# Performance work log

Measured on AMD Instinct MI355X. Metric: run time of the kernel, lower is better.

The kernel has to match this reference:

```python
import jax, jax.numpy as jnp
import numpy as np

IMG = 640
STRIDES = (8, 16, 32)
A = 5            # anchors per level
NC = 80          # num classes
IOU_TH = 0.5
NEG_RATIO = 1.0


def make_priors():
    scales = [1.0, 1.5, 2.0, 2.5, 3.0]
    out = []
    for s in STRIDES:
        f = IMG // s
        ys, xs = np.meshgrid(np.arange(f), np.arange(f), indexing='ij')
        cx = ((xs + 0.5) / f).ravel()
        cy = ((ys + 0.5) / f).ravel()
        for sc in scales:  # anchor-major to match merge_features (A, h, w) order
            wh = min(sc * 4.0 * s / IMG, 1.0)
            out.append(np.stack([cx, cy, np.full_like(cx, wh), np.full_like(cx, wh)], 1))
    return np.concatenate(out, 0).astype(np.float32)  # [42000, 4] cxcywh


def merge_features(feats):
    outs = []
    for feat in feats:
        n, c, h, w = feat.shape
        f = feat.reshape(n, A, c // A, h, w).transpose(0, 1, 3, 4, 2)
        outs.append(f.reshape(n, A * h * w, c // A))
    return jnp.concatenate(outs, axis=1)  # [n, M, 85]


def box_iou_cxcywh(a, b):
    # a [T,4], b [M,4] (cx,cy,w,h) -> IoU [T,M]
    a1 = jnp.concatenate([a[:, :2] - a[:, 2:] / 2, a[:, :2] + a[:, 2:] / 2], -1)
    b1 = jnp.concatenate([b[:, :2] - b[:, 2:] / 2, b[:, :2] + b[:, 2:] / 2], -1)
    tl = jnp.maximum(a1[:, None, :2], b1[None, :, :2])
    br = jnp.minimum(a1[:, None, 2:], b1[None, :, 2:])
    wh = jnp.clip(br - tl, 0.0)
    inter = wh[..., 0] * wh[..., 1]
    area_a = a[:, 2] * a[:, 3]
    area_b = b[:, 2] * b[:, 3]
    return inter / (area_a[:, None] + area_b[None, :] - inter + 1e-9)


def build_targets(targets, priors, batch):
    ious = box_iou_cxcywh(targets[:, 2:6], priors)  # [Nt, M]
    Nt, M = ious.shape
    img_ids = targets[:, 0].astype(jnp.int32)

    def per_image(i):
        valid = img_ids == i  # [Nt]
        iv = jnp.where(valid[:, None], ious, -1.0)
        best_gt_overlap = iv.max(0)            # [M]
        best_gt_idx = iv.argmax(0)             # [M]
        best_prior_idx = iv.argmax(1)          # [Nt]
        # torch: index_fill_(1) then sequential best_gt_overlap[best_prior_idx[j]] = j
        local_j = (jnp.cumsum(valid.astype(jnp.int32)) - 1).astype(jnp.float32)
        scat_idx = jnp.where(valid, best_prior_idx, M)  # drop invalid rows
        best_gt_overlap = best_gt_overlap.at[scat_idx].set(local_j, mode='drop')
        bbox = targets[best_gt_idx, 2:6]
        clss = targets[best_gt_idx, 1] + 1.0
        clss = jnp.where(best_gt_overlap < IOU_TH, 0.0, clss)
        t_xy = (bbox[:, :2] - priors[:, :2]) / priors[:, 2:]
        t_wh = jnp.log(bbox[:, 2:] / priors[:, 2:])
        return t_xy, t_wh, clss

    return jax.vmap(per_image)(jnp.arange(batch))  # [B,M,2],[B,M,2],[B,M]


def _smooth_l1(x):
    ax = jnp.abs(x)
    return jnp.where(ax < 1.0, 0.5 * ax * ax, ax - 0.5)


def compute_loss(preds, priors, targets):
    n, m, _ = preds.shape
    t_xy, t_wh, t_cls = build_targets(targets, priors, n)
    pos = t_cls > 0
    posf = pos.astype(preds.dtype)
    num_pos = posf.sum()

    # lbox: smooth L1 on xy and wh over positives (mean over pos*2 elements each)
    den2 = jnp.maximum(num_pos * 2.0, 1.0)
    lbox = (_smooth_l1(preds[..., 0:2] - t_xy) * posf[..., None]).sum() / den2 \
         + (_smooth_l1(preds[..., 2:4] - t_wh) * posf[..., None]).sum() / den2

    # lcls: cross entropy over positives, labels = t_cls - 1
    labels = jnp.clip(t_cls.astype(jnp.int32) - 1, 0, NC - 1)
    logz = jax.nn.log_softmax(preds[..., 5:], axis=-1)
    ce = -jnp.take_along_axis(logz, labels[..., None], axis=-1)[..., 0]
    lcls = (ce * posf).sum() / jnp.maximum(num_pos, 1.0)

    # hard negative mining (no grad): double argsort rank trick
    obj = preds[..., 4]
    loss_c = jax.lax.stop_gradient(-jax.nn.log_sigmoid(obj))
    loss_c = jnp.where(pos, 0.0, loss_c)
    order = jnp.argsort(-loss_c, axis=-1)
    rank = jnp.argsort(order, axis=-1)
    num_neg = jnp.minimum(NEG_RATIO * num_pos, m - num_pos)
    neg = rank.astype(preds.dtype) < num_neg
    sel = (pos | neg).astype(preds.dtype)

    # lobj: BCE-with-logits over pos|neg
    z = posf
    bce = jnp.maximum(obj, 0.0) - obj * z + jnp.log1p(jnp.exp(-jnp.abs(obj)))
    lobj = (bce * sel).sum() / jnp.maximum(sel.sum(), 1.0)

    loss = lbox + lcls + lobj
    return jnp.stack([loss, lbox, lobj, lcls])


def setup_inputs() -> dict:
    key = jax.random.key(0)
    ks = jax.random.split(key, 6)
    feat0 = jax.random.normal(ks[0], (8, 425, 80, 80), jnp.float32)
    feat1 = jax.random.normal(ks[1], (8, 425, 40, 40), jnp.float32)
    feat2 = jax.random.normal(ks[2], (8, 425, 20, 20), jnp.float32)
    B, T = 8, 20
    img = jnp.repeat(jnp.arange(B, dtype=jnp.float32), T)
    cls = jax.random.randint(ks[3], (B * T,), 0, NC).astype(jnp.float32)
    cxcy = jax.random.uniform(ks[4], (B * T, 2), minval=0.2, maxval=0.8)
    wh = jax.random.uniform(ks[5], (B * T, 2), minval=0.05, maxval=0.3)
    targets = jnp.concatenate([img[:, None], cls[:, None], cxcy, wh], 1)
    priors = jnp.asarray(make_priors())
    return {"feat0": feat0, "feat1": feat1, "feat2": feat2,
            "targets": targets, "priors": priors}


def reference(feat0, feat1, feat2, targets, priors):
    preds = merge_features([feat0, feat1, feat2])  # [8, 42000, 85]
    return compute_loss(preds, priors, targets)    # [loss, lbox, lobj, lcls]
```

## Files before the change

kernel.cpp:

```cpp
#include <hip/hip_runtime.h>
#include <math.h>

#define MTOT 42000
#define NB 8
#define NCLS 80
#define CAP_LIST 4096
#define NT_MAX 2048
#define GX_MAIN 165
#define NBLK_MAIN (GX_MAIN*NB)
#define NCHB 8
#define CSB 5250
#define TCH 512
#define TST 384

#define O_OVR 0
#define O_GIX (O_OVR + NB*MTOT*4)
#define O_LSC (O_GIX + NB*MTOT*4)
#define O_BCE (O_LSC + NB*MTOT*4)
#define O_LJ  (O_BCE + NB*MTOT*4)
#define O_BPP (((O_LJ + NT_MAX*4 + 7)/8)*8)
#define O_HP  (O_BPP + NT_MAX*NCHB*8)
#define O_HD  (O_HP + NBLK_MAIN*256*4)
#define O_PA  (O_HD + NB*256*4)
#define O_PN  (O_PA + NBLK_MAIN*16)
#define O_P2  (O_PN + NBLK_MAIN*4)
#define O_BINL (O_P2 + NBLK_MAIN*8)
#define O_HB  (((O_BINL + NB*CAP_LIST*2*4 + 255)/256)*256)
#define O_ACCI (O_HB + NB*256*4)
#define O_ZEND (O_ACCI + 128)
#define ZWORDS ((O_ZEND - O_HB)/4)
#define ZBLK ((ZWORDS + 255)/256)

__device__ __forceinline__ float iou_cxcywh(float acx,float acy,float aw,float ah,
                                            float bcx,float bcy,float bw,float bh){
  float ax0=acx-aw*0.5f, ay0=acy-ah*0.5f, ax1=acx+aw*0.5f, ay1=acy+ah*0.5f;
  float bx0=bcx-bw*0.5f, by0=bcy-bh*0.5f, bx1=bcx+bw*0.5f, by1=bcy+bh*0.5f;
  float tlx=fmaxf(ax0,bx0), tly=fmaxf(ay0,by0);
  float brx=fminf(ax1,bx1), bry=fminf(ay1,by1);
  float wx=fmaxf(brx-tlx,0.f), wy=fmaxf(bry-tly,0.f);
  float inter=wx*wy;
  return inter/(aw*ah+bw*bh-inter+1e-9f);
}

__device__ __forceinline__ float sl1(float x){
  float ax=fabsf(x); return ax<1.f ? 0.5f*ax*ax : ax-0.5f;
}

__device__ __forceinline__ void feat_base(const float* f0,const float* f1,const float* f2,
                                          int i,int m,const float** basep,int* hwp){
  const float* fp; int hw, loc;
  if(m<32000){ fp=f0; hw=6400; loc=m; }
  else if(m<40000){ fp=f1; hw=1600; loc=m-32000; }
  else { fp=f2; hw=400; loc=m-40000; }
  int a=loc/hw, p=loc-a*hw;
  *basep = fp + (size_t)(i*425 + a*85)*(size_t)hw + p;
  *hwp = hw;
}

__device__ __forceinline__ void fine_scan(const unsigned* hb,int ca,int kres,int* bs_out,int* r_out){
  if(ca==0x7fffffff){ *bs_out=0x7fffffff; *r_out=0; return; }
  int run=0, bs=-1, r=0;
  for(int f=255;f>=0;f--){
    int cb=(int)hb[f];
    if(run<kres && run+cb>=kres){ bs=(ca<<8)|f; r=kres-run; break; }
    run+=cb;
  }
  if(bs<0){ bs=(ca<<8); r=kres-run; }
  *bs_out=bs; *r_out=r;
}

__global__ void k_big0(const float* __restrict__ f0,const float* __restrict__ f1,const float* __restrict__ f2,
                       const float* __restrict__ tg,const float* __restrict__ priors,
                       int nt,int b0,int b1,
                       int* __restrict__ lj,unsigned* __restrict__ zbase,
                       float* __restrict__ ovr,int* __restrict__ gix,
                       float* __restrict__ lsc,float* __restrict__ bcearr,
                       unsigned* __restrict__ histP,int* __restrict__ partN,
                       unsigned long long* __restrict__ bpp){
  __shared__ float st[TCH*6];
  __shared__ float sc[TCH*4];
  __shared__ int cidx[TCH];
  __shared__ int s_ncomp;
  __shared__ unsigned long long su[256];
  __shared__ unsigned h[256];
  __shared__ int snp[4];
  int b=blockIdx.x, tid=threadIdx.x, lane=tid&63, wid=tid>>6;
  if(b<ZBLK){
    int w=b*256+tid;
    if(w<ZWORDS) zbase[w]=0u;
    return;
  }
  if(b<b0){
    int t=(b-ZBLK)*256+tid;
    if(t>=nt) return;
    int img=(int)tg[t*6];
    int j=0;
    for(int q=0;q<t;q++) if((int)tg[q*6]==img) j++;
    lj[t]=j;
    return;
  }
  if(b<b1){
    int idx=b-b0;
    int i=idx/GX_MAIN, cb=idx-(idx/GX_MAIN)*GX_MAIN;
    int m=cb*256+tid;
    bool valid=(m<MTOT);
    h[tid]=0u;
    const float* basep=f0; int hw=6400;
    float obj=0.f;
    if(valid){ feat_base(f0,f1,f2,i,m,&basep,&hw); obj=basep[(size_t)4*hw]; }
    float4 pr=make_float4(0.f,0.f,1.f,1.f);
    if(valid) pr=((const float4*)priors)[m];
    float maxv=-1.f; int bi=0;
    for(int base=0;base<nt;base+=TCH){
      int nch=min(TCH,nt-base);
      for(int j=tid;j<nch;j+=256){
        #pragma unroll
        for(int q=0;q<6;q++) st[j*6+q]=tg[(base+j)*6+q];
      }
      __syncthreads();
      if(tid<64){
        int cnt=0;
        for(int bb=0;bb<nch;bb+=64){
          int j=bb+tid;
          bool f=(j<nch)&&((int)st[j*6]==i);
          unsigned long long mk=__ballot(f);
          if(f){
            int pos=cnt+__popcll(mk&((1ull<<tid)-1ull));
            cidx[pos]=base+j;
            sc[pos*4+0]=st[j*6+2]; sc[pos*4+1]=st[j*6+3];
            sc[pos*4+2]=st[j*6+4]; sc[pos*4+3]=st[j*6+5];
          }
          cnt+=__popcll(mk);
        }
        if(tid==0) s_ncomp=cnt;
      }
      __syncthreads();
      int nci=s_ncomp;
      if(valid){
        for(int j=0;j<nci;j++){
          float v=iou_cxcywh(sc[j*4+0],sc[j*4+1],sc[j*4+2],sc[j*4+3],pr.x,pr.y,pr.z,pr.w);
          if(v>maxv){ maxv=v; bi=cidx[j]; }
        }
      }
      __syncthreads();
    }
    int npos=0;
    if(valid){
      int gid=i*MTOT+m;
      ovr[gid]=maxv; gix[gid]=bi;
      int gi=min(max(bi,0),nt-1);
      float tc=tg[gi*6+1]+1.f;
      bool pos=(maxv>=0.5f)&&(tc>0.f);
      float sp=log1pf(expf(-fabsf(obj)));
      float bce=fmaxf(obj,0.f)-(pos?obj:0.f)+sp;
      float lc=pos?0.f:(fmaxf(-obj,0.f)+sp);
      lsc[gid]=lc; bcearr[gid]=bce;
      atomicAdd(&h[__float_as_uint(lc)>>24],1u);
      npos=pos?1:0;
    }
    #pragma unroll
    for(int o=32;o>0;o>>=1) npos+=__shfl_xor(npos,o);
    if(lane==0) snp[wid]=npos;
    __syncthreads();
    histP[(size_t)idx*256+tid]=h[tid];
    if(tid==0) partN[idx]=snp[0]+snp[1]+snp[2]+snp[3];
  } else {
    int idx=b-b1;
    int t=idx/NCHB, c=idx-(idx/NCHB)*NCHB;
    float acx=tg[t*6+2],acy=tg[t*6+3],aw=tg[t*6+4],ah=tg[t*6+5];
    int m0=c*CSB, m1=min(m0+CSB,MTOT);
    float bv=-1.f; int bm=0;
    for(int m=m0+tid;m<m1;m+=256){
      float4 pr=((const float4*)priors)[m];
      float v=iou_cxcywh(acx,acy,aw,ah,pr.x,pr.y,pr.z,pr.w);
      if(v>bv){ bv=v; bm=m; }
    }
    unsigned long long p=(bv<0.f)?0ull
        :(((unsigned long long)__float_as_uint(bv))<<32)|(unsigned)(~bm);
    su[tid]=p;
    __syncthreads();
    for(int o=128;o>0;o>>=1){
      if(tid<o){ if(su[tid+o]>su[tid]) su[tid]=su[tid+o]; }
      __syncthreads();
    }
    if(tid==0) bpp[(size_t)t*NCHB+c]=su[0];
  }
}

__global__ void k_bpsc(const float* __restrict__ f0,const float* __restrict__ f1,const float* __restrict__ f2,
                       const float* __restrict__ tg,int nt,
                       const unsigned long long* __restrict__ bpp,
                       const int* __restrict__ lj,
                       float* __restrict__ ovr,const int* __restrict__ gix,
                       float* __restrict__ lsc,float* __restrict__ bcearr,
                       int* __restrict__ histD,int* __restrict__ acci){
  __shared__ int tbp[NT_MAX];
  __shared__ int timg[NT_MAX];
  __shared__ int hd[NB*256];
  __shared__ int npd;
  int tid=threadIdx.x;
  for(int e=tid;e<NB*256;e+=256) hd[e]=0;
  if(tid==0) npd=0;
  for(int t=tid;t<nt;t+=256){
    unsigned long long best=0ull;
    const unsigned long long* pp=&bpp[(size_t)t*NCHB];
    #pragma unroll
    for(int c=0;c<NCHB;c++){ unsigned long long v=pp[c]; if(v>best) best=v; }
    int bm=~((unsigned)(best&0xFFFFFFFFull));
    tbp[t]=min(max(bm,0),MTOT-1);
    timg[t]=(int)tg[t*6];
  }
  __syncthreads();
  for(int t=tid;t<nt;t+=256){
    int img=timg[t];
    if(img<0||img>=NB) continue;
    int myp=tbp[t];
    bool last=true;
    for(int q=t+1;q<nt;q++) if(timg[q]==img&&tbp[q]==myp){ last=false; break; }
    if(!last) continue;
    int gid=img*MTOT+myp;
    float ljv=(float)lj[t];
    float ov_old=ovr[gid];
    ovr[gid]=ljv;
    int gi=min(max(gix[gid],0),nt-1);
    float tc=tg[gi*6+1]+1.f;
    bool po=(ov_old>=0.5f)&&(tc>0.f);
    bool pn=(ljv>=0.5f)&&(tc>0.f);
    const float* basep; int hw;
    feat_base(f0,f1,f2,img,myp,&basep,&hw);
    float obj=basep[(size_t)4*hw];
    float sp=log1pf(expf(-fabsf(obj)));
    float bcen=fmaxf(obj,0.f)-(pn?obj:0.f)+sp;
    float lcn=pn?0.f:(fmaxf(-obj,0.f)+sp);
    float lco=lsc[gid];
    lsc[gid]=lcn; bcearr[gid]=bcen;
    atomicAdd(&hd[img*256+(int)(__float_as_uint(lco)>>24)],-1);
    atomicAdd(&hd[img*256+(int)(__float_as_uint(lcn)>>24)], 1);
    atomicAdd(&npd,(pn?1:0)-(po?1:0));
  }
  __syncthreads();
  for(int e=tid;e<NB*256;e+=256) histD[e]=hd[e];
  if(tid==0) acci[26]=npd;
}

__global__ void k_big2(const float* __restrict__ f0,const float* __restrict__ f1,const float* __restrict__ f2,
                       const float* __restrict__ tg,const float* __restrict__ priors,
                       const float* __restrict__ ovr,const int* __restrict__ gix,
                       const float* __restrict__ lsc,const float* __restrict__ bcearr,
                       const int* __restrict__ partN,const unsigned* __restrict__ histP,
                       const int* __restrict__ histD,int* __restrict__ acci,int nt,
                       unsigned* __restrict__ histB,float4* __restrict__ partA){
  __shared__ int an[256];
  __shared__ int hc[256];
  __shared__ unsigned hf[256];
  __shared__ int s_ca;
  __shared__ float rA[4],rB[4],rC[4],rD[4];
  int b=blockIdx.x, tid=threadIdx.x, lane=tid&63, wid=tid>>6;
  if(b<NBLK_MAIN){
    int i=b/GX_MAIN, cb=b-(b/GX_MAIN)*GX_MAIN;
    int n=0;
    for(int e=tid;e<NBLK_MAIN;e+=256) n+=partN[e];
    an[tid]=n;
    __syncthreads();
    for(int o=128;o>0;o>>=1){ if(tid<o) an[tid]+=an[tid+o]; __syncthreads(); }
    int np=an[0]+acci[26];
    int cbn=histD[i*256+tid];
    for(int blk=0;blk<GX_MAIN;blk++) cbn+=(int)histP[(size_t)(i*GX_MAIN+blk)*256+tid];
    hc[tid]=cbn;
    __syncthreads();
    if(tid==0){
      int kk=min(np,MTOT-np);
      int ca,kres;
      if(kk<=0){ ca=0x7fffffff; kres=0; }
      else{
        int run=0; ca=-1; kres=0;
        for(int c2=255;c2>=0;c2--){
          int x=hc[c2];
          if(run<kk&&run+x>=kk){ ca=c2; kres=kk-run; break; }
          run+=x;
        }
        if(ca<0){ ca=0; kres=kk-run; }
      }
      s_ca=ca;
      if(cb==0){ acci[2+i]=ca; acci[10+i]=kres; if(i==0) acci[0]=np; }
    }
    hf[tid]=0u;
    __syncthreads();
    int ca=s_ca;
    int m=cb*256+tid;
    if(m<MTOT && ca!=0x7fffffff){
      unsigned u=__float_as_uint(lsc[i*MTOT+m]);
      if((int)(u>>24)==ca) atomicAdd(&hf[(u>>16)&0xFF],1u);
    }
    __syncthreads();
    unsigned c=hf[tid];
    if(c) atomicAdd(&histB[i*256+tid],c);
  } else {
    int idx=b-NBLK_MAIN;
    int i=idx/GX_MAIN, cb=idx-(idx/GX_MAIN)*GX_MAIN;
    int m=cb*256+tid;
    bool valid=(m<MTOT);
    float lxy=0.f,lwh=0.f,bcep=0.f,wce=0.f;
    bool pos=false; int gi=0;
    if(valid){
      int gid=i*MTOT+m;
      float ov=ovr[gid];
      gi=min(max(gix[gid],0),nt-1);
      float tc=tg[gi*6+1]+1.f;
      pos=(ov>=0.5f)&&(tc>0.f);
      if(pos){
        const float* base; int hw;
        feat_base(f0,f1,f2,i,m,&base,&hw);
        bcep=bcearr[gid];
        float4 pr=((const float4*)priors)[m];
        float bx=tg[gi*6+2],by=tg[gi*6+3],bw=tg[gi*6+4],bh=tg[gi*6+5];
        float tx=(bx-pr.x)/pr.z, ty=(by-pr.y)/pr.w;
        float tw=logf(bw/pr.z), th=logf(bh/pr.w);
        lxy=sl1(base[0]-tx)+sl1(base[(size_t)hw]-ty);
        lwh=sl1(base[(size_t)2*hw]-tw)+sl1(base[(size_t)3*hw]-th);
      }
    }
    unsigned long long mask=__ballot(valid&&pos);
    while(mask){
      int s=__ffsll(mask)-1;
      mask&=mask-1;
      int m_s=__shfl(m,s);
      int gi_s=__shfl(gi,s);
      const float* bs2; int hws;
      feat_base(f0,f1,f2,i,m_s,&bs2,&hws);
      int label=(int)(tg[gi_s*6+1]+1.f)-1;
      label=min(NCLS-1,max(0,label));
      float v0=bs2[(size_t)(5+lane)*hws];
      float v1=(lane<16)?bs2[(size_t)(69+lane)*hws]:-3.0e38f;
      float mx=fmaxf(v0,v1);
      #pragma unroll
      for(int o=32;o>0;o>>=1) mx=fmaxf(mx,__shfl_xor(mx,o));
      float se=expf(v0-mx)+((lane<16)?expf(v1-mx):0.f);
      float xl=((lane==label)?v0:0.f)+((lane<16&&lane+64==label)?v1:0.f);
      #pragma unroll
      for(int o=32;o>0;o>>=1){ se+=__shfl_xor(se,o); xl+=__shfl_xor(xl,o); }
      wce+=logf(se)+mx-xl;
    }
    #pragma unroll
    for(int o=32;o>0;o>>=1){
      lxy+=__shfl_xor(lxy,o); lwh+=__shfl_xor(lwh,o); bcep+=__shfl_xor(bcep,o);
    }
    if(lane==0){ rA[wid]=lxy; rB[wid]=lwh; rC[wid]=wce; rD[wid]=bcep; }
    __syncthreads();
    if(tid==0)
      partA[idx]=make_float4(rA[0]+rA[1]+rA[2]+rA[3], rB[0]+rB[1]+rB[2]+rB[3],
                             rC[0]+rC[1]+rC[2]+rC[3], rD[0]+rD[1]+rD[2]+rD[3]);
  }
}

__global__ void k_select(const float* __restrict__ lsc,const float* __restrict__ bcearr,
                         const unsigned* __restrict__ histB,
                         int* __restrict__ acci,float2* __restrict__ part2,
                         int* __restrict__ binlist){
  __shared__ unsigned hb[256];
  __shared__ int sbs;
  __shared__ float ss[4]; __shared__ float sc2[4];
  int tid=threadIdx.x, lane=tid&63, wid=tid>>6;
  int i=blockIdx.y;
  int ca=acci[2+i], kres=acci[10+i];
  hb[tid]=(ca==0x7fffffff)?0u:histB[i*256+tid];
  __syncthreads();
  if(tid==0){ int bs,r; fine_scan(hb,ca,kres,&bs,&r); sbs=bs; }
  __syncthreads();
  int bs_=sbs;
  int m=blockIdx.x*256+tid;
  float s=0.f, c=0.f;
  if(m<MTOT){
    int gid=i*MTOT+m;
    unsigned u=__float_as_uint(lsc[gid]);
    int bin=(int)(u>>16);
    if(bin>bs_){ s=bcearr[gid]; c=1.f; }
    else if(bin==bs_){
      int idx=atomicAdd(&acci[18+i],1);
      if(idx<CAP_LIST){
        binlist[((size_t)i*CAP_LIST+idx)*2  ]=(int)u;
        binlist[((size_t)i*CAP_LIST+idx)*2+1]=gid;
      }
    }
  }
  #pragma unroll
  for(int o=32;o>0;o>>=1){ s+=__shfl_xor(s,o); c+=__shfl_xor(c,o); }
  if(lane==0){ ss[wid]=s; sc2[wid]=c; }
  __syncthreads();
  if(tid==0) part2[blockIdx.y*gridDim.x+blockIdx.x]=make_float2(ss[0]+ss[1]+ss[2]+ss[3], sc2[0]+sc2[1]+sc2[2]+sc2[3]);
}

__global__ void k_tiesfinal(const float* __restrict__ bcearr,const unsigned* __restrict__ histB,
                            int* __restrict__ acci,const int* __restrict__ binlist,
                            const float4* __restrict__ partA,const float2* __restrict__ part2,
                            float* __restrict__ out){
  __shared__ unsigned hb[NB*256];
  __shared__ int sbs[NB], sr2[NB];
  __shared__ int stg[NB*TST*2];
  __shared__ float tsumW[NB]; __shared__ float tcntW[NB];
  __shared__ float a0[512],a1[512],a2[512],a3[512],s0[512],s1[512];
  int tid=threadIdx.x, w=tid>>6, lane=tid&63;
  int ca=acci[2+w], kres=acci[10+w];
  for(int e=lane;e<256;e+=64) hb[w*256+e]=(ca==0x7fffffff)?0u:histB[w*256+e];
  __syncthreads();
  if(lane==0){ int bs,r; fine_scan(&hb[w*256],ca,kres,&bs,&r); sbs[w]=bs; sr2[w]=r; }
  __syncthreads();
  int bs=sbs[w], r=sr2[w];
  int n=min(acci[18+w],CAP_LIST);
  int nst=min(n,TST);
  if(bs!=0x7fffffff){
    for(int e=lane;e<nst;e+=64){
      stg[(w*TST+e)*2  ]=binlist[((size_t)w*CAP_LIST+e)*2  ];
      stg[(w*TST+e)*2+1]=binlist[((size_t)w*CAP_LIST+e)*2+1];
    }
  }
  __syncthreads();
  float tsum=0.f, tcnt=0.f;
  if(bs!=0x7fffffff){
    for(int e=lane;e<n;e+=64){
      unsigned ue; int ge;
      if(e<nst){ ue=(unsigned)stg[(w*TST+e)*2]; ge=stg[(w*TST+e)*2+1]; }
      else{ ue=(unsigned)binlist[((size_t)w*CAP_LIST+e)*2]; ge=binlist[((size_t)w*CAP_LIST+e)*2+1]; }
      int rank=0;
      for(int q=0;q<n;q++){
        unsigned uq; int gq;
        if(q<nst){ uq=(unsigned)stg[(w*TST+q)*2]; gq=stg[(w*TST+q)*2+1]; }
        else{ uq=(unsigned)binlist[((size_t)w*CAP_LIST+q)*2]; gq=binlist[((size_t)w*CAP_LIST+q)*2+1]; }
        rank += ((uq>ue)||(uq==ue&&gq<ge))?1:0;
      }
      if(rank<r){ tsum+=bcearr[ge]; tcnt+=1.f; }
    }
  }
  #pragma unroll
  for(int o=32;o>0;o>>=1){ tsum+=__shfl_xor(tsum,o); tcnt+=__shfl_xor(tcnt,o); }
  if(lane==0){ tsumW[w]=tsum; tcntW[w]=tcnt; }
  __syncthreads();
  float x=0,y=0,z=0,ww=0,ns=0,nc=0;
  for(int e=tid;e<NBLK_MAIN;e+=512){
    float4 p=partA[e]; x+=p.x; y+=p.y; z+=p.z; ww+=p.w;
    float2 q=part2[e]; ns+=q.x; nc+=q.y;
  }
  a0[tid]=x; a1[tid]=y; a2[tid]=z; a3[tid]=ww; s0[tid]=ns; s1[tid]=nc;
  __syncthreads();
  for(int o=256;o>0;o>>=1){
    if(tid<o){
      a0[tid]+=a0[tid+o]; a1[tid]+=a1[tid+o]; a2[tid]+=a2[tid+o]; a3[tid]+=a3[tid+o];
      s0[tid]+=s0[tid+o]; s1[tid]+=s1[tid+o];
    }
    __syncthreads();
  }
  if(tid==0){
    float negsum=s0[0], negcnt=s1[0];
    for(int im=0;im<NB;im++){ negsum+=tsumW[im]; negcnt+=tcntW[im]; }
    int np=acci[0];
    float npf=(float)np;
    float den2=fmaxf(2.f*npf,1.f);
    float lbox=a0[0]/den2+a1[0]/den2;
    float lcls=a2[0]/fmaxf(npf,1.f);
    float selc=npf+negcnt;
    float lobj=(a3[0]+negsum)/fmaxf(selc,1.f);
    out[0]=lbox+lcls+lobj;
    out[1]=lbox;
    out[2]=lobj;
    out[3]=lcls;
  }
}

extern "C" void kernel_launch(void* const* d_in, const int* in_sizes, int n_in,
                              void* d_out, int out_size, void* d_ws, size_t ws_size,
                              hipStream_t stream) {
  const float* f0=(const float*)d_in[0];
  const float* f1=(const float*)d_in[1];
  const float* f2=(const float*)d_in[2];
  const float* tg=(const float*)d_in[3];
  const float* priors=(const float*)d_in[4];
  int nt = in_sizes[3]/6;
  if(nt>NT_MAX) nt=NT_MAX;
  if(nt<1) nt=1;

  char* ws=(char*)d_ws;
  float*    ovr    =(float*)   (ws+O_OVR);
  int*      gix    =(int*)     (ws+O_GIX);
  float*    lsc    =(float*)   (ws+O_LSC);
  float*    bcearr =(float*)   (ws+O_BCE);
  int*      lj     =(int*)     (ws+O_LJ);
  unsigned long long* bpp=(unsigned long long*)(ws+O_BPP);
  unsigned* histP  =(unsigned*)(ws+O_HP);
  int*      histD  =(int*)     (ws+O_HD);
  float4*   partA  =(float4*)  (ws+O_PA);
  int*      partN  =(int*)     (ws+O_PN);
  float2*   part2  =(float2*)  (ws+O_P2);
  int*      binlist=(int*)     (ws+O_BINL);
  unsigned* histB  =(unsigned*)(ws+O_HB);
  int*      acci   =(int*)     (ws+O_ACCI);
  unsigned* zbase  =(unsigned*)(ws+O_HB);

  int ntb=(nt+255)/256;
  int b0=ZBLK+ntb, b1=b0+NBLK_MAIN;
  k_big0<<<b1+nt*NCHB,256,0,stream>>>(f0,f1,f2,tg,priors,nt,b0,b1,lj,zbase,ovr,gix,lsc,bcearr,histP,partN,bpp);
  k_bpsc<<<1,256,0,stream>>>(f0,f1,f2,tg,nt,bpp,lj,ovr,gix,lsc,bcearr,histD,acci);
  k_big2<<<2*NBLK_MAIN,256,0,stream>>>(f0,f1,f2,tg,priors,ovr,gix,lsc,bcearr,partN,histP,histD,acci,nt,histB,partA);
  dim3 gm(GX_MAIN, NB);
  k_select<<<gm,256,0,stream>>>(lsc,bcearr,histB,acci,part2,binlist);
  k_tiesfinal<<<1,512,0,stream>>>(bcearr,histB,acci,binlist,partA,part2,(float*)d_out);
}
```

Baseline: 131.0 us.

## Compute per-image histogram threshold once in single-block kernel instead of every block

The reduction of per-block class histograms and positive counts, plus the threshold bin search for hard negative mining, moves out of each of the 1320 k_big2 blocks into the single-block k_bpsc kernel. k_big2 now reads only the precomputed threshold from acci. This removes redundant global reads (165x256 histogram entries and the partN array per block) and a serial scan repeated in every block. The cost is that this work is now serialized in one 256-thread block, which lengthens that kernel's critical path.

```diff
diff --git a/kernel.cpp b/kernel.cpp
--- a/kernel.cpp
+++ b/kernel.cpp
@@ -20,8 +20,7 @@
 #define O_LJ  (O_BCE + NB*MTOT*4)
 #define O_BPP (((O_LJ + NT_MAX*4 + 7)/8)*8)
 #define O_HP  (O_BPP + NT_MAX*NCHB*8)
-#define O_HD  (O_HP + NBLK_MAIN*256*4)
-#define O_PA  (O_HD + NB*256*4)
+#define O_PA  (O_HP + NBLK_MAIN*256*4)
 #define O_PN  (O_PA + NBLK_MAIN*16)
 #define O_P2  (O_PN + NBLK_MAIN*4)
 #define O_BINL (O_P2 + NBLK_MAIN*8)
@@ -193,10 +192,12 @@
                        const int* __restrict__ lj,
                        float* __restrict__ ovr,const int* __restrict__ gix,
                        float* __restrict__ lsc,float* __restrict__ bcearr,
-                       int* __restrict__ histD,int* __restrict__ acci){
+                       const unsigned* __restrict__ histP,const int* __restrict__ partN,
+                       int* __restrict__ acci){
   __shared__ int tbp[NT_MAX];
   __shared__ int timg[NT_MAX];
   __shared__ int hd[NB*256];
+  __shared__ int an[256];
   __shared__ int npd;
   int tid=threadIdx.x;
   for(int e=tid;e<NB*256;e+=256) hd[e]=0;
@@ -239,54 +240,50 @@
     atomicAdd(&npd,(pn?1:0)-(po?1:0));
   }
   __syncthreads();
-  for(int e=tid;e<NB*256;e+=256) histD[e]=hd[e];
-  if(tid==0) acci[26]=npd;
+  for(int img=0;img<NB;img++){
+    int s=0;
+    #pragma unroll 4
+    for(int blk=0;blk<GX_MAIN;blk++) s+=(int)histP[(size_t)(img*GX_MAIN+blk)*256+tid];
+    hd[img*256+tid]+=s;
+  }
+  int n=0;
+  for(int e=tid;e<NBLK_MAIN;e+=256) n+=partN[e];
+  an[tid]=n;
+  __syncthreads();
+  for(int o=128;o>0;o>>=1){ if(tid<o) an[tid]+=an[tid+o]; __syncthreads(); }
+  int np=an[0]+npd;
+  if(tid==0) acci[0]=np;
+  if(tid<NB){
+    int i=tid;
+    int kk=min(np,MTOT-np);
+    if(kk<=0){ acci[2+i]=0x7fffffff; acci[10+i]=0; }
+    else{
+      int run=0, ca=-1, kres=0;
+      for(int c2=255;c2>=0;c2--){
+        int x=hd[i*256+c2];
+        if(run<kk&&run+x>=kk){ ca=c2; kres=kk-run; break; }
+        run+=x;
+      }
+      if(ca<0){ ca=0; kres=kk-run; }
+      acci[2+i]=ca; acci[10+i]=kres;
+    }
+  }
 }
 
 __global__ void k_big2(const float* __restrict__ f0,const float* __restrict__ f1,const float* __restrict__ f2,
                        const float* __restrict__ tg,const float* __restrict__ priors,
                        const float* __restrict__ ovr,const int* __restrict__ gix,
                        const float* __restrict__ lsc,const float* __restrict__ bcearr,
-                       const int* __restrict__ partN,const unsigned* __restrict__ histP,
-                       const int* __restrict__ histD,int* __restrict__ acci,int nt,
+                       const int* __restrict__ acci,int nt,
                        unsigned* __restrict__ histB,float4* __restrict__ partA){
-  __shared__ int an[256];
-  __shared__ int hc[256];
   __shared__ unsigned hf[256];
-  __shared__ int s_ca;
   __shared__ float rA[4],rB[4],rC[4],rD[4];
   int b=blockIdx.x, tid=threadIdx.x, lane=tid&63, wid=tid>>6;
   if(b<NBLK_MAIN){
     int i=b/GX_MAIN, cb=b-(b/GX_MAIN)*GX_MAIN;
-    int n=0;
-    for(int e=tid;e<NBLK_MAIN;e+=256) n+=partN[e];
-    an[tid]=n;
-    __syncthreads();
-    for(int o=128;o>0;o>>=1){ if(tid<o) an[tid]+=an[tid+o]; __syncthreads(); }
-    int np=an[0]+acci[26];
-    int cbn=histD[i*256+tid];
-    for(int blk=0;blk<GX_MAIN;blk++) cbn+=(int)histP[(size_t)(i*GX_MAIN+blk)*256+tid];
-    hc[tid]=cbn;
-    __syncthreads();
-    if(tid==0){
-      int kk=min(np,MTOT-np);
-      int ca,kres;
-      if(kk<=0){ ca=0x7fffffff; kres=0; }
-      else{
-        int run=0; ca=-1; kres=0;
-        for(int c2=255;c2>=0;c2--){
-          int x=hc[c2];
-          if(run<kk&&run+x>=kk){ ca=c2; kres=kk-run; break; }
-          run+=x;
-        }
-        if(ca<0){ ca=0; kres=kk-run; }
-      }
-      s_ca=ca;
-      if(cb==0){ acci[2+i]=ca; acci[10+i]=kres; if(i==0) acci[0]=np; }
-    }
+    int ca=acci[2+i];
     hf[tid]=0u;
     __syncthreads();
-    int ca=s_ca;
     int m=cb*256+tid;
     if(m<MTOT && ca!=0x7fffffff){
       unsigned u=__float_as_uint(lsc[i*MTOT+m]);
@@ -486,7 +483,6 @@
   int*      lj     =(int*)     (ws+O_LJ);
   unsigned long long* bpp=(unsigned long long*)(ws+O_BPP);
   unsigned* histP  =(unsigned*)(ws+O_HP);
-  int*      histD  =(int*)     (ws+O_HD);
   float4*   partA  =(float4*)  (ws+O_PA);
   int*      partN  =(int*)     (ws+O_PN);
   float2*   part2  =(float2*)  (ws+O_P2);
@@ -498,8 +494,8 @@
   int ntb=(nt+255)/256;
   int b0=ZBLK+ntb, b1=b0+NBLK_MAIN;
   k_big0<<<b1+nt*NCHB,256,0,stream>>>(f0,f1,f2,tg,priors,nt,b0,b1,lj,zbase,ovr,gix,lsc,bcearr,histP,partN,bpp);
-  k_bpsc<<<1,256,0,stream>>>(f0,f1,f2,tg,nt,bpp,lj,ovr,gix,lsc,bcearr,histD,acci);
-  k_big2<<<2*NBLK_MAIN,256,0,stream>>>(f0,f1,f2,tg,priors,ovr,gix,lsc,bcearr,partN,histP,histD,acci,nt,histB,partA);
+  k_bpsc<<<1,256,0,stream>>>(f0,f1,f2,tg,nt,bpp,lj,ovr,gix,lsc,bcearr,histP,partN,acci);
+  k_big2<<<2*NBLK_MAIN,256,0,stream>>>(f0,f1,f2,tg,priors,ovr,gix,lsc,bcearr,acci,nt,histB,partA);
   dim3 gm(GX_MAIN, NB);
   k_select<<<gm,256,0,stream>>>(lsc,bcearr,histB,acci,part2,binlist);
   k_tiesfinal<<<1,512,0,stream>>>(bcearr,histB,acci,binlist,partA,part2,(float*)d_out);
```

Result: slower. 234.8 us (+79.2%).
